# Kernel tuning notes

Hardware: AMD Instinct MI355X
Metric: run time of the kernel (lower is better)

The kernel has to match this reference:

```python
import jax, jax.numpy as jnp
import numpy as np

N_NODES = 100000
N_EDGES = 3200000
HID = 16
MP_ROUNDS = 3


def _mlp(w1, b1, w2, b2, x):
    # channels-first MLP applied per edge/node: x is [C_in, E]
    h = jax.nn.relu(w1 @ x + b1[:, None])
    return w2 @ h + b2[:, None]


def setup_inputs() -> dict:
    key = jax.random.key(0)
    ks = jax.random.split(key, 20)
    s = lambda k, shp: jax.random.normal(k, shp, dtype=jnp.float32) * 0.1
    inp = {
        "nodes": jax.random.normal(ks[0], (N_NODES,), dtype=jnp.float32),
        "edges_init": jax.random.normal(ks[1], (N_EDGES,), dtype=jnp.float32),
        "senders": jax.random.randint(ks[2], (N_EDGES,), 0, N_NODES, dtype=jnp.int32),
        "receivers": jax.random.randint(ks[3], (N_EDGES,), 0, N_NODES, dtype=jnp.int32),
        # EdgeEncoder: 1 -> HID -> HID
        "enc_w1": s(ks[4], (HID, 1)), "enc_b1": jnp.zeros((HID,), jnp.float32),
        "enc_w2": s(ks[5], (HID, HID)), "enc_b2": jnp.zeros((HID,), jnp.float32),
        # Node update MLP: (1 + 2*HID) -> HID -> 1  (shared across rounds)
        "node_w1": s(ks[6], (HID, 1 + 2 * HID)), "node_b1": jnp.zeros((HID,), jnp.float32),
        "node_w2": s(ks[7], (1, HID)), "node_b2": jnp.zeros((1,), jnp.float32),
        # Edge update MLP: (HID + 2) -> HID -> HID  (shared across rounds)
        "edge_w1": s(ks[8], (HID, HID + 2)), "edge_b1": jnp.zeros((HID,), jnp.float32),
        "edge_w2": s(ks[9], (HID, HID)), "edge_b2": jnp.zeros((HID,), jnp.float32),
        # EdgeDecoder: HID -> HID -> 1
        "dec_w1": s(ks[10], (HID, HID)), "dec_b1": jnp.zeros((HID,), jnp.float32),
        "dec_w2": s(ks[11], (1, HID)), "dec_b2": jnp.zeros((1,), jnp.float32),
        "alpha": jnp.float32(0.1),
    }
    return inp


def reference(nodes, edges_init, senders, receivers,
              enc_w1, enc_b1, enc_w2, enc_b2,
              node_w1, node_b1, node_w2, node_b2,
              edge_w1, edge_b1, edge_w2, edge_b2,
              dec_w1, dec_b1, dec_w2, dec_b2, alpha):
    n_nodes = nodes.shape[0]
    norm = jnp.abs(edges_init).max()
    e = edges_init / norm                      # [E]
    e = _mlp(enc_w1, enc_b1, enc_w2, enc_b2, e[None, :])   # [HID, E]
    for _ in range(MP_ROUNDS):                 # shared-weight MP blocks
        # gather/scatter: aggregate edge features to nodes
        agg_s = jax.ops.segment_sum(e.T, senders, num_segments=n_nodes).T     # [HID, N]
        agg_r = jax.ops.segment_sum(e.T, receivers, num_segments=n_nodes).T   # [HID, N]
        node_in = jnp.concatenate([nodes[None, :], agg_s, agg_r], axis=0)     # [1+2H, N]
        nodes = _mlp(node_w1, node_b1, node_w2, node_b2, node_in)[0]          # [N]
        edge_in = jnp.concatenate([e, nodes[senders][None, :], nodes[receivers][None, :]], axis=0)  # [H+2, E]
        e = _mlp(edge_w1, edge_b1, edge_w2, edge_b2, edge_in)                 # [HID, E]
    e = _mlp(dec_w1, dec_b1, dec_w2, dec_b2, e)[0]          # [E]
    low_tri_data = edges_init + alpha * (e * norm)          # L = L + alpha*GNN(L)
    return low_tri_data
```

## Files before the change

kernel.cpp:

```cpp
#include <hip/hip_runtime.h>
#include <hip/hip_bf16.h>

#define N_NODES 100000
#define N_EDGES 3200000
#define HID 16
#define MAXDEG 128
#define NPART 8
#define PART_NODES (N_NODES / NPART)

static constexpr int BLK = 256;

__device__ __forceinline__ float frelu(float x) { return fmaxf(x, 0.f); }
__device__ __forceinline__ float bf2f(unsigned short u) {
  return __uint_as_float(((unsigned int)u) << 16);
}

union E16 {
  float4 f4[2];
  __hip_bfloat16 h[16];
};

__global__ __launch_bounds__(256) void k_norm(const float* __restrict__ edges,
                                              unsigned int* __restrict__ normbits) {
  float m = 0.f;
  for (int i = blockIdx.x * blockDim.x + threadIdx.x; i < N_EDGES;
       i += gridDim.x * blockDim.x)
    m = fmaxf(m, fabsf(edges[i]));
#pragma unroll
  for (int off = 32; off > 0; off >>= 1)
    m = fmaxf(m, __shfl_down(m, off, 64));
  __shared__ float smax[BLK / 64];
  if ((threadIdx.x & 63) == 0) smax[threadIdx.x >> 6] = m;
  __syncthreads();
  if (threadIdx.x == 0) {
    float b = smax[0];
#pragma unroll
    for (int w = 1; w < BLK / 64; ++w) b = fmaxf(b, smax[w]);
    atomicMax(normbits, __float_as_uint(b));
  }
}

__global__ __launch_bounds__(256) void k_build(const int* __restrict__ senders,
                                               const int* __restrict__ receivers,
                                               int* __restrict__ count,
                                               int* __restrict__ ell) {
  int p = blockIdx.x & (NPART - 1);
  int q = blockIdx.x >> 3;
  int nblk = gridDim.x >> 3;
  int lo = p * PART_NODES, hi = lo + PART_NODES;
  for (int i = q * blockDim.x + threadIdx.x; i < N_EDGES;
       i += nblk * blockDim.x) {
    int s = senders[i];
    if (s >= lo && s < hi) {
      int slot = atomicAdd(&count[s], 1);
      if (slot < MAXDEG) ell[(size_t)s * MAXDEG + slot] = (i << 1);
    }
    int r = receivers[i];
    if (r >= lo && r < hi) {
      int slot = atomicAdd(&count[r], 1);
      if (slot < MAXDEG) ell[(size_t)r * MAXDEG + slot] = (i << 1) | 1;
    }
  }
}

__global__ __launch_bounds__(256) void k_encode(
    const float* __restrict__ edges, const float* __restrict__ w1,
    const float* __restrict__ b1, const float* __restrict__ w2,
    const float* __restrict__ b2, const unsigned int* __restrict__ normbits,
    __hip_bfloat16* __restrict__ e) {
  int i = blockIdx.x * blockDim.x + threadIdx.x;
  if (i >= N_EDGES) return;
  float norm = __uint_as_float(*normbits);
  float x = edges[i] / norm;
  float h[HID];
#pragma unroll
  for (int j = 0; j < HID; ++j) h[j] = frelu(fmaf(w1[j], x, b1[j]));
  E16 o;
#pragma unroll
  for (int j = 0; j < HID; ++j) {
    float acc = b2[j];
#pragma unroll
    for (int k = 0; k < HID; ++k) acc = fmaf(w2[j * HID + k], h[k], acc);
    o.h[j] = __float2bfloat16(acc);
  }
  float4* ep = (float4*)(e + (size_t)i * HID);
  ep[0] = o.f4[0];
  ep[1] = o.f4[1];
}

__global__ __launch_bounds__(256) void k_gather(
    const unsigned short* __restrict__ e, const int* __restrict__ count,
    const int* __restrict__ ell, float* __restrict__ agg) {
  int wave = (blockIdx.x * blockDim.x + threadIdx.x) >> 6;
  int lane = threadIdx.x & 63;
  int half = lane >> 5;
  int l32 = lane & 31;
  int sub = l32 & 3;
  int j8 = l32 >> 2;
  int n = wave * 2 + half;
  if (n >= N_NODES) return;
  int deg = count[n];
  if (deg > MAXDEG) deg = MAXDEG;
  const int* lst = ell + (size_t)n * MAXDEG;
  int ent0 = __builtin_nontemporal_load(lst + l32);
  int ent1 = __builtin_nontemporal_load(lst + 32 + l32);
  float as[4] = {0.f, 0.f, 0.f, 0.f};
  float ar[4] = {0.f, 0.f, 0.f, 0.f};
#pragma unroll
  for (int t = 0; t < 8; ++t) {
    int slot = t * 8 + j8;
    int entry = __shfl(t < 4 ? ent0 : ent1, half * 32 + (t & 3) * 8 + j8, 64);
    bool ok = slot < deg;
    int edge = ok ? (entry >> 1) : 0;
    ushort4 raw = *(const ushort4*)(e + (size_t)edge * HID + sub * 4);
    float v[4] = {bf2f(raw.x), bf2f(raw.y), bf2f(raw.z), bf2f(raw.w)};
    bool recv = ok && (entry & 1);
    bool send = ok && !(entry & 1);
#pragma unroll
    for (int c = 0; c < 4; ++c) {
      as[c] += send ? v[c] : 0.f;
      ar[c] += recv ? v[c] : 0.f;
    }
  }
  if (__any(deg > 64)) {
    int ent2 = __builtin_nontemporal_load(lst + 64 + l32);
    int ent3 = __builtin_nontemporal_load(lst + 96 + l32);
#pragma unroll
    for (int t = 0; t < 8; ++t) {
      int slot = 64 + t * 8 + j8;
      int entry = __shfl(t < 4 ? ent2 : ent3, half * 32 + (t & 3) * 8 + j8, 64);
      bool ok = slot < deg;
      int edge = ok ? (entry >> 1) : 0;
      ushort4 raw = *(const ushort4*)(e + (size_t)edge * HID + sub * 4);
      float v[4] = {bf2f(raw.x), bf2f(raw.y), bf2f(raw.z), bf2f(raw.w)};
      bool recv = ok && (entry & 1);
      bool send = ok && !(entry & 1);
#pragma unroll
      for (int c = 0; c < 4; ++c) {
        as[c] += send ? v[c] : 0.f;
        ar[c] += recv ? v[c] : 0.f;
      }
    }
  }
#pragma unroll
  for (int off = 16; off >= 4; off >>= 1) {
#pragma unroll
    for (int c = 0; c < 4; ++c) {
      as[c] += __shfl_down(as[c], off, 64);
      ar[c] += __shfl_down(ar[c], off, 64);
    }
  }
  if (l32 < 4) {
    *(float4*)(agg + (size_t)n * 32 + l32 * 4) =
        make_float4(as[0], as[1], as[2], as[3]);
    *(float4*)(agg + (size_t)n * 32 + 16 + l32 * 4) =
        make_float4(ar[0], ar[1], ar[2], ar[3]);
  }
}

__global__ __launch_bounds__(256) void k_node(
    const float* __restrict__ nodes_in, const float* __restrict__ agg,
    const float* __restrict__ w1, const float* __restrict__ b1,
    const float* __restrict__ w2, const float* __restrict__ b2,
    float* __restrict__ nodes_out) {
  int n = blockIdx.x * blockDim.x + threadIdx.x;
  if (n >= N_NODES) return;
  float x0 = nodes_in[n];
  const float4* ap = (const float4*)(agg + (size_t)n * 32);
  float av[32];
#pragma unroll
  for (int q = 0; q < 8; ++q) {
    float4 v = ap[q];
    av[q * 4 + 0] = v.x;
    av[q * 4 + 1] = v.y;
    av[q * 4 + 2] = v.z;
    av[q * 4 + 3] = v.w;
  }
  float out = b2[0];
#pragma unroll
  for (int j = 0; j < HID; ++j) {
    float acc = fmaf(w1[j * 33], x0, b1[j]);
#pragma unroll
    for (int k = 0; k < 32; ++k) acc = fmaf(w1[j * 33 + 1 + k], av[k], acc);
    out = fmaf(w2[j], frelu(acc), out);
  }
  nodes_out[n] = out;
}

__global__ __launch_bounds__(256) void k_edge(
    __hip_bfloat16* __restrict__ e, const int* __restrict__ senders,
    const int* __restrict__ receivers, const float* __restrict__ nodes,
    const float* __restrict__ w1, const float* __restrict__ b1,
    const float* __restrict__ w2, const float* __restrict__ b2) {
  int i = blockIdx.x * blockDim.x + threadIdx.x;
  if (i >= N_EDGES) return;
  int s = senders[i], r = receivers[i];
  float ns = nodes[s], nr = nodes[r];
  float4* ep = (float4*)(e + (size_t)i * HID);
  E16 in;
  in.f4[0] = ep[0];
  in.f4[1] = ep[1];
  float x[HID];
#pragma unroll
  for (int k = 0; k < HID; ++k) x[k] = __bfloat162float(in.h[k]);
  float h[HID];
#pragma unroll
  for (int j = 0; j < HID; ++j) {
    float acc = b1[j];
#pragma unroll
    for (int k = 0; k < HID; ++k) acc = fmaf(w1[j * 18 + k], x[k], acc);
    acc = fmaf(w1[j * 18 + 16], ns, acc);
    acc = fmaf(w1[j * 18 + 17], nr, acc);
    h[j] = frelu(acc);
  }
  E16 o;
#pragma unroll
  for (int j = 0; j < HID; ++j) {
    float acc = b2[j];
#pragma unroll
    for (int k = 0; k < HID; ++k) acc = fmaf(w2[j * HID + k], h[k], acc);
    o.h[j] = __float2bfloat16(acc);
  }
  ep[0] = o.f4[0];
  ep[1] = o.f4[1];
}

__global__ __launch_bounds__(256) void k_final(
    const __hip_bfloat16* __restrict__ e, const int* __restrict__ senders,
    const int* __restrict__ receivers, const float* __restrict__ nodes,
    const float* __restrict__ w1, const float* __restrict__ b1,
    const float* __restrict__ w2, const float* __restrict__ b2,
    const float* __restrict__ dw1, const float* __restrict__ db1,
    const float* __restrict__ dw2, const float* __restrict__ db2,
    const float* __restrict__ edges_init,
    const unsigned int* __restrict__ normbits, const float* __restrict__ alpha,
    float* __restrict__ out) {
  int i = blockIdx.x * blockDim.x + threadIdx.x;
  if (i >= N_EDGES) return;
  int s = senders[i], r = receivers[i];
  float ns = nodes[s], nr = nodes[r];
  const float4* ep = (const float4*)(e + (size_t)i * HID);
  E16 in;
  in.f4[0] = ep[0];
  in.f4[1] = ep[1];
  float x[HID];
#pragma unroll
  for (int k = 0; k < HID; ++k) x[k] = __bfloat162float(in.h[k]);
  float h[HID];
#pragma unroll
  for (int j = 0; j < HID; ++j) {
    float acc = b1[j];
#pragma unroll
    for (int k = 0; k < HID; ++k) acc = fmaf(w1[j * 18 + k], x[k], acc);
    acc = fmaf(w1[j * 18 + 16], ns, acc);
    acc = fmaf(w1[j * 18 + 17], nr, acc);
    h[j] = frelu(acc);
  }
  float e3[HID];
#pragma unroll
  for (int j = 0; j < HID; ++j) {
    float acc = b2[j];
#pragma unroll
    for (int k = 0; k < HID; ++k) acc = fmaf(w2[j * HID + k], h[k], acc);
    e3[j] = acc;
  }
  float d = db2[0];
#pragma unroll
  for (int j = 0; j < HID; ++j) {
    float acc = db1[j];
#pragma unroll
    for (int k = 0; k < HID; ++k) acc = fmaf(dw1[j * HID + k], e3[k], acc);
    d = fmaf(dw2[j], frelu(acc), d);
  }
  float norm = __uint_as_float(*normbits);
  out[i] = fmaf(alpha[0], d * norm, edges_init[i]);
}

extern "C" void kernel_launch(void* const* d_in, const int* in_sizes, int n_in,
                              void* d_out, int out_size, void* d_ws,
                              size_t ws_size, hipStream_t stream) {
  const float* nodes0 = (const float*)d_in[0];
  const float* edges0 = (const float*)d_in[1];
  const int* senders = (const int*)d_in[2];
  const int* receivers = (const int*)d_in[3];
  const float* enc_w1 = (const float*)d_in[4];
  const float* enc_b1 = (const float*)d_in[5];
  const float* enc_w2 = (const float*)d_in[6];
  const float* enc_b2 = (const float*)d_in[7];
  const float* node_w1 = (const float*)d_in[8];
  const float* node_b1 = (const float*)d_in[9];
  const float* node_w2 = (const float*)d_in[10];
  const float* node_b2 = (const float*)d_in[11];
  const float* edge_w1 = (const float*)d_in[12];
  const float* edge_b1 = (const float*)d_in[13];
  const float* edge_w2 = (const float*)d_in[14];
  const float* edge_b2 = (const float*)d_in[15];
  const float* dec_w1 = (const float*)d_in[16];
  const float* dec_b1 = (const float*)d_in[17];
  const float* dec_w2 = (const float*)d_in[18];
  const float* dec_b2 = (const float*)d_in[19];
  const float* alpha = (const float*)d_in[20];

  char* ws = (char*)d_ws;
  __hip_bfloat16* e = (__hip_bfloat16*)ws;
  float* agg = (float*)(ws + (size_t)N_EDGES * HID * 2);
  float* nb1 = agg + (size_t)N_NODES * 32;
  float* nb2 = nb1 + N_NODES;
  unsigned int* normbits = (unsigned int*)(nb2 + N_NODES);
  int* count = (int*)(normbits + 16);
  int* ell = count + N_NODES;

  const int egrid = N_EDGES / BLK;
  const int ngrid = (N_NODES + BLK - 1) / BLK;
  const int ggrid = N_NODES / 8;
  const int bgrid = 3520;

  hipMemsetAsync(normbits, 0, sizeof(unsigned int), stream);
  hipMemsetAsync(count, 0, (size_t)N_NODES * sizeof(int), stream);
  k_norm<<<512, BLK, 0, stream>>>(edges0, normbits);
  k_build<<<bgrid, BLK, 0, stream>>>(senders, receivers, count, ell);
  k_encode<<<egrid, BLK, 0, stream>>>(edges0, enc_w1, enc_b1, enc_w2, enc_b2,
                                      normbits, e);
  k_gather<<<ggrid, BLK, 0, stream>>>((const unsigned short*)e, count, ell, agg);
  k_node<<<ngrid, BLK, 0, stream>>>(nodes0, agg, node_w1, node_b1, node_w2,
                                    node_b2, nb1);
  k_edge<<<egrid, BLK, 0, stream>>>(e, senders, receivers, nb1, edge_w1,
                                    edge_b1, edge_w2, edge_b2);
  k_gather<<<ggrid, BLK, 0, stream>>>((const unsigned short*)e, count, ell, agg);
  k_node<<<ngrid, BLK, 0, stream>>>(nb1, agg, node_w1, node_b1, node_w2,
                                    node_b2, nb2);
  k_edge<<<egrid, BLK, 0, stream>>>(e, senders, receivers, nb2, edge_w1,
                                    edge_b1, edge_w2, edge_b2);
  k_gather<<<ggrid, BLK, 0, stream>>>((const unsigned short*)e, count, ell, agg);
  k_node<<<ngrid, BLK, 0, stream>>>(nb2, agg, node_w1, node_b1, node_w2,
                                    node_b2, nb1);
  k_final<<<egrid, BLK, 0, stream>>>(e, senders, receivers, nb1, edge_w1,
                                     edge_b1, edge_w2, edge_b2, dec_w1, dec_b1,
                                     dec_w2, dec_b2, edges0, normbits, alpha,
                                     (float*)d_out);
}
```

Baseline: 1.030 ms.

## Replace atomic ELL build with two-pass bucketed split and per-bucket CSR sort

The padded per-node ELL adjacency, which was built with global atomics scattered across many blocks, is replaced by a two-stage build. The first stage bins edge endpoints into 256 node buckets through shared-memory FIFOs and flushes them to global memory in chunks. The second stage sorts each bucket in shared memory into a compact CSR list with per-node offsets and degrees. The gather kernel now reads these compact offsets, which should improve locality of the adjacency reads and cut scattered global atomics. The bucket buffer reuses the edge-feature workspace before encoding, and fixed capacities (PCAP, LCAP) risk silent truncation on skewed inputs.

```diff
diff --git a/kernel.cpp b/kernel.cpp
--- a/kernel.cpp
+++ b/kernel.cpp
@@ -5,8 +5,11 @@
 #define N_EDGES 3200000
 #define HID 16
 #define MAXDEG 128
-#define NPART 8
-#define PART_NODES (N_NODES / NPART)
+#define NB 256
+#define NPB 391
+#define PCAP 28672
+#define FDEPTH 48
+#define LCAP 26624
 
 static constexpr int BLK = 256;
 
@@ -40,26 +43,135 @@
   }
 }
 
-__global__ __launch_bounds__(256) void k_build(const int* __restrict__ senders,
-                                               const int* __restrict__ receivers,
-                                               int* __restrict__ count,
-                                               int* __restrict__ ell) {
-  int p = blockIdx.x & (NPART - 1);
-  int q = blockIdx.x >> 3;
-  int nblk = gridDim.x >> 3;
-  int lo = p * PART_NODES, hi = lo + PART_NODES;
-  for (int i = q * blockDim.x + threadIdx.x; i < N_EDGES;
-       i += nblk * blockDim.x) {
-    int s = senders[i];
-    if (s >= lo && s < hi) {
-      int slot = atomicAdd(&count[s], 1);
-      if (slot < MAXDEG) ell[(size_t)s * MAXDEG + slot] = (i << 1);
-    }
-    int r = receivers[i];
-    if (r >= lo && r < hi) {
-      int slot = atomicAdd(&count[r], 1);
-      if (slot < MAXDEG) ell[(size_t)r * MAXDEG + slot] = (i << 1) | 1;
-    }
+__global__ __launch_bounds__(1024) void k_split(const int* __restrict__ senders,
+                                                const int* __restrict__ receivers,
+                                                int* __restrict__ gcnt,
+                                                unsigned int* __restrict__ pairs) {
+  __shared__ __align__(16) unsigned int fifo[NB][FDEPTH];
+  __shared__ int fcnt[NB];
+  const int t = threadIdx.x;
+  if (t < NB) fcnt[t] = 0;
+  __syncthreads();
+  const int e0 = blockIdx.x * (N_EDGES / 256);
+  const int e1 = e0 + (N_EDGES / 256);
+  for (int base = e0; base < e1; base += 1024) {
+    const int i = base + t;
+    if (i < e1) {
+      int s = senders[i];
+      unsigned int bs = (unsigned int)s / NPB;
+      unsigned int us = (((unsigned int)s - bs * NPB) << 23) | ((unsigned int)i << 1);
+      int pos = atomicAdd(&fcnt[bs], 1);
+      if (pos < FDEPTH) {
+        fifo[bs][pos] = us;
+      } else {
+        int gb = atomicAdd(&gcnt[bs], 1);
+        if (gb < PCAP) pairs[(size_t)bs * PCAP + gb] = us;
+      }
+      int r = receivers[i];
+      unsigned int br = (unsigned int)r / NPB;
+      unsigned int ur = (((unsigned int)r - br * NPB) << 23) | ((unsigned int)i << 1) | 1u;
+      pos = atomicAdd(&fcnt[br], 1);
+      if (pos < FDEPTH) {
+        fifo[br][pos] = ur;
+      } else {
+        int gb = atomicAdd(&gcnt[br], 1);
+        if (gb < PCAP) pairs[(size_t)br * PCAP + gb] = ur;
+      }
+    }
+    __syncthreads();
+    const bool last = (base + 1024 >= e1);
+    if (t < NB) {
+      int c = fcnt[t];
+      if (c > FDEPTH) c = FDEPTH;
+      int nf = last ? c : (c & ~15);
+      if (nf > 0) {
+        int gb = atomicAdd(&gcnt[t], nf);
+        unsigned int* dst = pairs + (size_t)t * PCAP + gb;
+        if ((gb & 3) == 0 && gb + nf <= PCAP) {
+          int k = 0;
+          for (; k + 4 <= nf; k += 4)
+            *(uint4*)(dst + k) = *(const uint4*)(&fifo[t][k]);
+          for (; k < nf; ++k) dst[k] = fifo[t][k];
+        } else {
+          for (int k = 0; k < nf; ++k)
+            if (gb + k < PCAP) dst[k] = fifo[t][k];
+        }
+        int res = c - nf;
+        for (int k = 0; k < res; ++k) fifo[t][k] = fifo[t][nf + k];
+        fcnt[t] = res;
+      } else {
+        fcnt[t] = c;
+      }
+    }
+    __syncthreads();
+  }
+}
+
+__global__ __launch_bounds__(1024) void k_bsort(const unsigned int* __restrict__ pairs,
+                                                const int* __restrict__ gcnt,
+                                                int* __restrict__ ell,
+                                                int* __restrict__ off,
+                                                int* __restrict__ deg) {
+  __shared__ unsigned int sorted[LCAP];
+  __shared__ int hist[NPB + 1];
+  __shared__ int pref[NPB + 1];
+  __shared__ int sc[NPB];
+  __shared__ int cur[NPB];
+  const int b = blockIdx.x;
+  const int t = threadIdx.x;
+  const int nt = blockDim.x;
+  int nb = gcnt[b];
+  if (nb > PCAP) nb = PCAP;
+  const unsigned int* P = pairs + (size_t)b * PCAP;
+  for (int k = t; k <= NPB; k += nt) hist[k] = 0;
+  __syncthreads();
+  for (int i = t; i < nb; i += nt) atomicAdd(&hist[P[i] >> 23], 1);
+  __syncthreads();
+  if (t < NPB) {
+    int c = hist[t];
+    sc[t] = (c > MAXDEG) ? MAXDEG : c;
+  }
+  __syncthreads();
+  if (t < NPB) hist[t] = sc[t];
+  for (int d = 1; d < NPB; d <<= 1) {
+    int add = 0;
+    if (t < NPB && t >= d) add = sc[t - d];
+    __syncthreads();
+    if (t < NPB && t >= d) sc[t] += add;
+    __syncthreads();
+  }
+  if (t < NPB) pref[t] = sc[t] - hist[t];
+  if (t == 0) pref[NPB] = sc[NPB - 1];
+  __syncthreads();
+  const int node0 = b * NPB;
+  for (int k = t; k < NPB; k += nt) {
+    int n = node0 + k;
+    if (n < N_NODES) {
+      off[n] = b * PCAP + pref[k];
+      deg[n] = hist[k];
+    }
+  }
+  int nlo = 0;
+  while (nlo < NPB) {
+    const int base0 = pref[nlo];
+    int nhi = nlo;
+    while (nhi < NPB && pref[nhi + 1] - base0 <= LCAP) ++nhi;
+    for (int k = nlo + t; k < nhi; k += nt) cur[k] = pref[k] - base0;
+    __syncthreads();
+    for (int i = t; i < nb; i += nt) {
+      unsigned int u = P[i];
+      int nl = u >> 23;
+      if (nl >= nlo && nl < nhi) {
+        int p = atomicAdd(&cur[nl], 1);
+        if (p < pref[nl] - base0 + hist[nl]) sorted[p] = u & 0x7FFFFFu;
+      }
+    }
+    __syncthreads();
+    const int csz = pref[nhi] - base0;
+    int* dst = ell + (size_t)b * PCAP + base0;
+    for (int i = t; i < csz; i += nt) dst[i] = (int)sorted[i];
+    __syncthreads();
+    nlo = nhi;
   }
 }
 
@@ -89,8 +201,9 @@
 }
 
 __global__ __launch_bounds__(256) void k_gather(
-    const unsigned short* __restrict__ e, const int* __restrict__ count,
-    const int* __restrict__ ell, float* __restrict__ agg) {
+    const unsigned short* __restrict__ e, const int* __restrict__ offp,
+    const int* __restrict__ degp, const int* __restrict__ ell,
+    float* __restrict__ agg) {
   int wave = (blockIdx.x * blockDim.x + threadIdx.x) >> 6;
   int lane = threadIdx.x & 63;
   int half = lane >> 5;
@@ -99,9 +212,9 @@
   int j8 = l32 >> 2;
   int n = wave * 2 + half;
   if (n >= N_NODES) return;
-  int deg = count[n];
+  int deg = degp[n];
   if (deg > MAXDEG) deg = MAXDEG;
-  const int* lst = ell + (size_t)n * MAXDEG;
+  const int* lst = ell + offp[n];
   int ent0 = __builtin_nontemporal_load(lst + l32);
   int ent1 = __builtin_nontemporal_load(lst + 32 + l32);
   float as[4] = {0.f, 0.f, 0.f, 0.f};
@@ -303,35 +416,38 @@
 
   char* ws = (char*)d_ws;
   __hip_bfloat16* e = (__hip_bfloat16*)ws;
+  unsigned int* pairs = (unsigned int*)ws;
   float* agg = (float*)(ws + (size_t)N_EDGES * HID * 2);
   float* nb1 = agg + (size_t)N_NODES * 32;
   float* nb2 = nb1 + N_NODES;
   unsigned int* normbits = (unsigned int*)(nb2 + N_NODES);
-  int* count = (int*)(normbits + 16);
-  int* ell = count + N_NODES;
+  int* deg = (int*)(normbits + 16);
+  int* off = deg + N_NODES;
+  int* gcnt = off + N_NODES;
+  int* ell = gcnt + NB;
 
   const int egrid = N_EDGES / BLK;
   const int ngrid = (N_NODES + BLK - 1) / BLK;
   const int ggrid = N_NODES / 8;
-  const int bgrid = 3520;
 
   hipMemsetAsync(normbits, 0, sizeof(unsigned int), stream);
-  hipMemsetAsync(count, 0, (size_t)N_NODES * sizeof(int), stream);
+  hipMemsetAsync(gcnt, 0, NB * sizeof(int), stream);
   k_norm<<<512, BLK, 0, stream>>>(edges0, normbits);
-  k_build<<<bgrid, BLK, 0, stream>>>(senders, receivers, count, ell);
+  k_split<<<256, 1024, 0, stream>>>(senders, receivers, gcnt, pairs);
+  k_bsort<<<NB, 1024, 0, stream>>>(pairs, gcnt, ell, off, deg);
   k_encode<<<egrid, BLK, 0, stream>>>(edges0, enc_w1, enc_b1, enc_w2, enc_b2,
                                       normbits, e);
-  k_gather<<<ggrid, BLK, 0, stream>>>((const unsigned short*)e, count, ell, agg);
+  k_gather<<<ggrid, BLK, 0, stream>>>((const unsigned short*)e, off, deg, ell, agg);
   k_node<<<ngrid, BLK, 0, stream>>>(nodes0, agg, node_w1, node_b1, node_w2,
                                     node_b2, nb1);
   k_edge<<<egrid, BLK, 0, stream>>>(e, senders, receivers, nb1, edge_w1,
                                     edge_b1, edge_w2, edge_b2);
-  k_gather<<<ggrid, BLK, 0, stream>>>((const unsigned short*)e, count, ell, agg);
+  k_gather<<<ggrid, BLK, 0, stream>>>((const unsigned short*)e, off, deg, ell, agg);
   k_node<<<ngrid, BLK, 0, stream>>>(nb1, agg, node_w1, node_b1, node_w2,
                                     node_b2, nb2);
   k_edge<<<egrid, BLK, 0, stream>>>(e, senders, receivers, nb2, edge_w1,
                                     edge_b1, edge_w2, edge_b2);
-  k_gather<<<ggrid, BLK, 0, stream>>>((const unsigned short*)e, count, ell, agg);
+  k_gather<<<ggrid, BLK, 0, stream>>>((const unsigned short*)e, off, deg, ell, agg);
   k_node<<<ngrid, BLK, 0, stream>>>(nb2, agg, node_w1, node_b1, node_w2,
                                     node_b2, nb1);
   k_final<<<egrid, BLK, 0, stream>>>(e, senders, receivers, nb1, edge_w1,
```

Result: faster. 880.5 us (-14.6%).
